# Optimization experiments

Measured on AMD Instinct MI355X. Metric: run time of the kernel, lower is better.

## Reference

```python
import jax, jax.numpy as jnp
import numpy as np
from math import sqrt

MEM_SIZE = 1024
MEM_DIM = 256


def setup_inputs() -> dict:
    key = jax.random.key(0)
    k1, k2, k3 = jax.random.split(key, 3)
    x = jax.random.normal(k1, (8, 256, 64, 64), dtype=jnp.float32)
    mask = jax.random.randint(k2, (8, 1, 64, 64), 0, 2).astype(jnp.bool_)
    mem = jax.random.normal(k3, (1, MEM_DIM, MEM_SIZE), dtype=jnp.float32)
    return {"x": x, "mask": mask, "mem": mem}


def reference(x, mask, mem):
    # masked-detach blend: x.detach() * ~mask + x * mask
    x = jnp.where(mask, x, jax.lax.stop_gradient(x))
    B, K, H, W = x.shape
    xf = x.reshape(B, K, H * W)            # (B, K, N)
    m = mem[0]                              # (K, M) with M = mem_size
    # logits = m_key @ x / sqrt(K)  -> (B, M, N)
    logits = jnp.einsum('km,bkn->bmn', m, xf) / sqrt(K)
    attn = jax.nn.softmax(logits, axis=1)   # softmax over memory axis
    # out = m @ attn -> (B, K, N)
    out = jnp.einsum('km,bmn->bkn', m, attn).reshape(B, K, H, W)
    return (out, logits)
```

## Files before the change

### kernel.cpp

```cpp
#include <hip/hip_runtime.h>
#include <stdint.h>


typedef __attribute__((ext_vector_type(8))) __bf16 bf16x8;
typedef __attribute__((ext_vector_type(4))) float f32x4;

#define BQ 8
#define KD 256
#define MD 1024
#define ND 4096
#define NT 64

__device__ __forceinline__ unsigned short bf16_rne(float f) {
    union { float f; uint32_t u; } c; c.f = f;
    uint32_t u = c.u;
    uint32_t r = (u + 0x7FFFu + ((u >> 16) & 1u)) >> 16;
    return (unsigned short)r;
}

__global__ void prep_mem(const float* __restrict__ mem,
                         unsigned short* __restrict__ mT,
                         unsigned short* __restrict__ mR) {
    const int k = blockIdx.x;
    const int t = threadIdx.x;
    float4 v = reinterpret_cast<const float4*>(mem + (size_t)k * MD)[t];
    unsigned short h0 = bf16_rne(v.x), h1 = bf16_rne(v.y),
                   h2 = bf16_rne(v.z), h3 = bf16_rne(v.w);
    reinterpret_cast<uint2*>(mR + (size_t)k * MD)[t] =
        make_uint2((uint32_t)h0 | ((uint32_t)h1 << 16),
                   (uint32_t)h2 | ((uint32_t)h3 << 16));
    const int mm = t * 4;
    mT[(size_t)(mm + 0) * KD + k] = h0;
    mT[(size_t)(mm + 1) * KD + k] = h1;
    mT[(size_t)(mm + 2) * KD + k] = h2;
    mT[(size_t)(mm + 3) * KD + k] = h3;
}

__global__ __launch_bounds__(1024, 4) void fused_attn_mem(
    const float* __restrict__ x,
    const unsigned short* __restrict__ mT,
    const unsigned short* __restrict__ mR,
    float* __restrict__ out,
    float* __restrict__ logits)
{
    extern __shared__ char lds[];
    float* red_max = (float*)(lds);
    float* red_sum = (float*)(lds + 4096);

    const int tid = threadIdx.x;
    const int w   = tid >> 6;
    const int l   = tid & 63;
    const int l15 = l & 15;
    const int l4  = l >> 4;

    const int bid = blockIdx.x;
    const int g   = bid & 7;
    const int j   = bid >> 3;
    const int strip = g * 8 + (j & 7);
    const int b     = j >> 3;
    const int n0    = strip * NT;

    {
        const float* xb = x + (size_t)b * KD * ND + n0;
        const int k  = tid >> 2;
        const int nh = (tid & 3) * 16;
        const float4* src = reinterpret_cast<const float4*>(xb + (size_t)k * ND + nh);
        float4 v0 = src[0], v1 = src[1], v2 = src[2], v3 = src[3];
        float vals[16] = {v0.x, v0.y, v0.z, v0.w, v1.x, v1.y, v1.z, v1.w,
                          v2.x, v2.y, v2.z, v2.w, v3.x, v3.y, v3.z, v3.w};
        #pragma unroll
        for (int jj = 0; jj < 16; ++jj) {
            const int n = nh + jj;
            const int off = n * 512 + (((k >> 3) ^ (n & 7)) << 4) + (k & 7) * 2;
            *(unsigned short*)(lds + off) = bf16_rne(vals[jj]);
        }
    }
    __syncthreads();

    f32x4 acc[4][4];
    #pragma unroll
    for (int rt = 0; rt < 4; ++rt)
        #pragma unroll
        for (int ct = 0; ct < 4; ++ct)
            acc[rt][ct] = (f32x4){0.f, 0.f, 0.f, 0.f};

    #pragma unroll
    for (int ks = 0; ks < 8; ++ks) {
        const int kk = ks * 32 + l4 * 8;
        bf16x8 bfr[4];
        #pragma unroll
        for (int ct = 0; ct < 4; ++ct) {
            const int n = ct * 16 + l15;
            const int off = n * 512 + (((kk >> 3) ^ (n & 7)) << 4);
            bfr[ct] = *(const bf16x8*)(lds + off);
        }
        #pragma unroll
        for (int rt = 0; rt < 4; ++rt) {
            const int row = w * 64 + rt * 16 + l15;
            const bf16x8 afr = *(const bf16x8*)(mT + (size_t)row * KD + kk);
            #pragma unroll
            for (int ct = 0; ct < 4; ++ct)
                acc[rt][ct] = __builtin_amdgcn_mfma_f32_16x16x32_bf16(afr, bfr[ct], acc[rt][ct], 0, 0, 0);
        }
    }

    float lmax[4] = {-3e38f, -3e38f, -3e38f, -3e38f};
    #pragma unroll
    for (int rt = 0; rt < 4; ++rt) {
        #pragma unroll
        for (int ct = 0; ct < 4; ++ct) {
            f32x4 v = acc[rt][ct] * 0.0625f;
            acc[rt][ct] = v;
            lmax[ct] = fmaxf(lmax[ct], fmaxf(fmaxf(v[0], v[1]), fmaxf(v[2], v[3])));
        }
    }

    {
        char* sw = lds + 32768 + w * 4608;
        float* lg = logits + (size_t)b * MD * ND + n0;
        #pragma unroll
        for (int rt = 0; rt < 4; ++rt) {
            #pragma unroll
            for (int ct = 0; ct < 4; ++ct) {
                const int n = ct * 16 + l15;
                #pragma unroll
                for (int r = 0; r < 4; ++r) {
                    const int mloc = l4 * 4 + r;
                    *(float*)(sw + mloc * 272 + n * 4) = acc[rt][ct][r];
                }
            }
            __asm__ volatile("s_waitcnt lgkmcnt(0)" ::: "memory");
            __builtin_amdgcn_sched_barrier(0);
            #pragma unroll
            for (int p = 0; p < 4; ++p) {
                const int mloc = p * 4 + l4;
                const f32x4 v = *(const f32x4*)(sw + mloc * 272 + l15 * 16);
                *(f32x4*)(lg + (size_t)(w * 64 + rt * 16 + mloc) * ND + l15 * 4) = v;
            }
            __asm__ volatile("s_waitcnt lgkmcnt(0)" ::: "memory");
            __builtin_amdgcn_sched_barrier(0);
        }
    }

    #pragma unroll
    for (int ct = 0; ct < 4; ++ct) {
        float m = lmax[ct];
        m = fmaxf(m, __shfl_xor(m, 16, 64));
        m = fmaxf(m, __shfl_xor(m, 32, 64));
        lmax[ct] = m;
    }
    __syncthreads();
    if (l < 16) {
        #pragma unroll
        for (int ct = 0; ct < 4; ++ct)
            red_max[(w * 4 + ct) * 16 + l] = lmax[ct];
    }
    __syncthreads();

    float cmax[4];
    #pragma unroll
    for (int ct = 0; ct < 4; ++ct) {
        float m = -3e38f;
        #pragma unroll
        for (int ww = 0; ww < 16; ++ww)
            m = fmaxf(m, red_max[(ww * 4 + ct) * 16 + l15]);
        cmax[ct] = m;
    }

    float lsum[4] = {0.f, 0.f, 0.f, 0.f};
    #pragma unroll
    for (int rt = 0; rt < 4; ++rt) {
        #pragma unroll
        for (int ct = 0; ct < 4; ++ct) {
            f32x4 v = acc[rt][ct];
            v[0] = __expf(v[0] - cmax[ct]);
            v[1] = __expf(v[1] - cmax[ct]);
            v[2] = __expf(v[2] - cmax[ct]);
            v[3] = __expf(v[3] - cmax[ct]);
            lsum[ct] += (v[0] + v[1]) + (v[2] + v[3]);
            acc[rt][ct] = v;
        }
    }
    #pragma unroll
    for (int ct = 0; ct < 4; ++ct) {
        float s = lsum[ct];
        s += __shfl_xor(s, 16, 64);
        s += __shfl_xor(s, 32, 64);
        lsum[ct] = s;
    }
    if (l < 16) {
        #pragma unroll
        for (int ct = 0; ct < 4; ++ct)
            red_sum[(w * 4 + ct) * 16 + l] = lsum[ct];
    }
    __syncthreads();

    float rs[4];
    #pragma unroll
    for (int ct = 0; ct < 4; ++ct) {
        float s = 0.f;
        #pragma unroll
        for (int ww = 0; ww < 16; ++ww)
            s += red_sum[(ww * 4 + ct) * 16 + l15];
        rs[ct] = 1.0f / s;
    }

    #pragma unroll
    for (int rt = 0; rt < 4; ++rt) {
        #pragma unroll
        for (int ct = 0; ct < 4; ++ct) {
            f32x4 v = acc[rt][ct];
            unsigned short h0 = bf16_rne(v[0] * rs[ct]);
            unsigned short h1 = bf16_rne(v[1] * rs[ct]);
            unsigned short h2 = bf16_rne(v[2] * rs[ct]);
            unsigned short h3 = bf16_rne(v[3] * rs[ct]);
            const int m0 = w * 64 + rt * 16 + l4 * 4;
            const int n  = ct * 16 + l15;
            const int off = 32768 + n * 2048 + (((m0 >> 3) ^ (n & 7)) << 4) + (m0 & 7) * 2;
            *(uint2*)(lds + off) = make_uint2((uint32_t)h0 | ((uint32_t)h1 << 16),
                                              (uint32_t)h2 | ((uint32_t)h3 << 16));
        }
    }
    __syncthreads();

    f32x4 acc2[4];
    #pragma unroll
    for (int ct = 0; ct < 4; ++ct)
        acc2[ct] = (f32x4){0.f, 0.f, 0.f, 0.f};

    const unsigned short* arow = mR + (size_t)(w * 16 + l15) * MD;
    #pragma unroll 4
    for (int ks = 0; ks < 32; ++ks) {
        const int mk = ks * 32 + l4 * 8;
        const bf16x8 a2 = *(const bf16x8*)(arow + mk);
        #pragma unroll
        for (int ct = 0; ct < 4; ++ct) {
            const int n = ct * 16 + l15;
            const int off = 32768 + n * 2048 + (((mk >> 3) ^ (n & 7)) << 4);
            const bf16x8 b2 = *(const bf16x8*)(lds + off);
            acc2[ct] = __builtin_amdgcn_mfma_f32_16x16x32_bf16(a2, b2, acc2[ct], 0, 0, 0);
        }
    }
    __syncthreads();

    {
        char* sw = lds + 32768 + w * 4608;
        float* ob = out + (size_t)b * KD * ND + n0;
        #pragma unroll
        for (int ct = 0; ct < 4; ++ct) {
            const int n = ct * 16 + l15;
            #pragma unroll
            for (int r = 0; r < 4; ++r) {
                const int rr = l4 * 4 + r;
                *(float*)(sw + rr * 272 + n * 4) = acc2[ct][r];
            }
        }
        __asm__ volatile("s_waitcnt lgkmcnt(0)" ::: "memory");
        __builtin_amdgcn_sched_barrier(0);
        #pragma unroll
        for (int p = 0; p < 4; ++p) {
            const int rr = p * 4 + l4;
            const f32x4 v = *(const f32x4*)(sw + rr * 272 + l15 * 16);
            *(f32x4*)(ob + (size_t)(w * 16 + rr) * ND + l15 * 4) = v;
        }
    }
}

extern "C" void kernel_launch(void* const* d_in, const int* in_sizes, int n_in,
                              void* d_out, int out_size, void* d_ws, size_t ws_size,
                              hipStream_t stream) {
    (void)in_sizes; (void)n_in; (void)out_size; (void)ws_size;
    const float* x   = (const float*)d_in[0];
    const float* mem = (const float*)d_in[2];

    float* out    = (float*)d_out;
    float* logits = (float*)d_out + (size_t)BQ * KD * ND;

    unsigned short* mT = (unsigned short*)d_ws;
    unsigned short* mR = mT + (size_t)MD * KD;

    static int lds_attr_set = 0;
    if (!lds_attr_set) {
        hipFuncSetAttribute(reinterpret_cast<const void*>(&fused_attn_mem),
                            hipFuncAttributeMaxDynamicSharedMemorySize, 163840);
        lds_attr_set = 1;
    }

    prep_mem<<<dim3(256), dim3(256), 0, stream>>>(mem, mT, mR);
    fused_attn_mem<<<dim3(BQ * (ND / NT)), dim3(1024), 163840, stream>>>(x, mT, mR, out, logits);
}
```

Baseline: 112.1 us.

## Widen column tile to 128 with two-pass attention GEMM and reorganized LDS

Doubles the per-block column tile from 64 to 128, halving the grid and halving how often each block re-reads the bf16 memory matrices from global/L2. The second GEMM now runs in two passes over halves of the memory axis so the bf16 attention tile fits in LDS. The max reduction moves ahead of the logits store, x is loaded with nontemporal loads, and the logits/out writes use 32-wide coalesced rows. In exchange, the accumulator array doubles in size, which raises register pressure and may cause spills, and the extra pass adds barriers.

```diff
diff --git a/kernel.cpp b/kernel.cpp
--- a/kernel.cpp
+++ b/kernel.cpp
@@ -9,7 +9,12 @@
 #define KD 256
 #define MD 1024
 #define ND 4096
-#define NT 64
+#define NT 128
+
+#define SCR_STRIDE 8448
+#define SCR_ROW    528
+#define RED_MAX_OFF 147456
+#define RED_SUM_OFF 155648
 
 __device__ __forceinline__ unsigned short bf16_rne(float f) {
     union { float f; uint32_t u; } c; c.f = f;
@@ -44,8 +49,8 @@
     float* __restrict__ logits)
 {
     extern __shared__ char lds[];
-    float* red_max = (float*)(lds);
-    float* red_sum = (float*)(lds + 4096);
+    float* red_max = (float*)(lds + RED_MAX_OFF);
+    float* red_sum = (float*)(lds + RED_SUM_OFF);
 
     const int tid = threadIdx.x;
     const int w   = tid >> 6;
@@ -53,43 +58,46 @@
     const int l15 = l & 15;
     const int l4  = l >> 4;
 
-    const int bid = blockIdx.x;
-    const int g   = bid & 7;
-    const int j   = bid >> 3;
-    const int strip = g * 8 + (j & 7);
-    const int b     = j >> 3;
-    const int n0    = strip * NT;
+    const int q   = blockIdx.x;
+    const int g   = q & 7;
+    const int j   = q >> 3;
+    const int b   = j >> 2;
+    const int sid = g * 4 + (j & 3);
+    const int n0  = sid * NT;
+
+    const float* xb = x + (size_t)b * KD * ND + n0;
+    float* lg = logits + (size_t)b * MD * ND + n0;
+    float* ob = out + (size_t)b * KD * ND + n0;
 
     {
-        const float* xb = x + (size_t)b * KD * ND + n0;
         const int k  = tid >> 2;
-        const int nh = (tid & 3) * 16;
-        const float4* src = reinterpret_cast<const float4*>(xb + (size_t)k * ND + nh);
-        float4 v0 = src[0], v1 = src[1], v2 = src[2], v3 = src[3];
-        float vals[16] = {v0.x, v0.y, v0.z, v0.w, v1.x, v1.y, v1.z, v1.w,
-                          v2.x, v2.y, v2.z, v2.w, v3.x, v3.y, v3.z, v3.w};
-        #pragma unroll
-        for (int jj = 0; jj < 16; ++jj) {
+        const int nh = (tid & 3) * 32;
+        const f32x4* src = reinterpret_cast<const f32x4*>(xb + (size_t)k * ND + nh);
+        f32x4 v[8];
+        #pragma unroll
+        for (int i = 0; i < 8; ++i) v[i] = __builtin_nontemporal_load(src + i);
+        #pragma unroll
+        for (int jj = 0; jj < 32; ++jj) {
             const int n = nh + jj;
             const int off = n * 512 + (((k >> 3) ^ (n & 7)) << 4) + (k & 7) * 2;
-            *(unsigned short*)(lds + off) = bf16_rne(vals[jj]);
+            *(unsigned short*)(lds + off) = bf16_rne(v[jj >> 2][jj & 3]);
         }
     }
     __syncthreads();
 
-    f32x4 acc[4][4];
+    f32x4 acc[4][8];
     #pragma unroll
     for (int rt = 0; rt < 4; ++rt)
         #pragma unroll
-        for (int ct = 0; ct < 4; ++ct)
+        for (int ct = 0; ct < 8; ++ct)
             acc[rt][ct] = (f32x4){0.f, 0.f, 0.f, 0.f};
 
     #pragma unroll
     for (int ks = 0; ks < 8; ++ks) {
         const int kk = ks * 32 + l4 * 8;
-        bf16x8 bfr[4];
-        #pragma unroll
-        for (int ct = 0; ct < 4; ++ct) {
+        bf16x8 bfr[8];
+        #pragma unroll
+        for (int ct = 0; ct < 8; ++ct) {
             const int n = ct * 16 + l15;
             const int off = n * 512 + (((kk >> 3) ^ (n & 7)) << 4);
             bfr[ct] = *(const bf16x8*)(lds + off);
@@ -99,79 +107,81 @@
             const int row = w * 64 + rt * 16 + l15;
             const bf16x8 afr = *(const bf16x8*)(mT + (size_t)row * KD + kk);
             #pragma unroll
-            for (int ct = 0; ct < 4; ++ct)
+            for (int ct = 0; ct < 8; ++ct)
                 acc[rt][ct] = __builtin_amdgcn_mfma_f32_16x16x32_bf16(afr, bfr[ct], acc[rt][ct], 0, 0, 0);
         }
     }
 
-    float lmax[4] = {-3e38f, -3e38f, -3e38f, -3e38f};
+    float lmax[8];
+    #pragma unroll
+    for (int ct = 0; ct < 8; ++ct) lmax[ct] = -3e38f;
     #pragma unroll
     for (int rt = 0; rt < 4; ++rt) {
         #pragma unroll
-        for (int ct = 0; ct < 4; ++ct) {
+        for (int ct = 0; ct < 8; ++ct) {
             f32x4 v = acc[rt][ct] * 0.0625f;
             acc[rt][ct] = v;
             lmax[ct] = fmaxf(lmax[ct], fmaxf(fmaxf(v[0], v[1]), fmaxf(v[2], v[3])));
         }
     }
+    #pragma unroll
+    for (int ct = 0; ct < 8; ++ct) {
+        float m = lmax[ct];
+        m = fmaxf(m, __shfl_xor(m, 16, 64));
+        m = fmaxf(m, __shfl_xor(m, 32, 64));
+        lmax[ct] = m;
+    }
+    if (l < 16) {
+        #pragma unroll
+        for (int ct = 0; ct < 8; ++ct)
+            red_max[(w * 8 + ct) * 16 + l] = lmax[ct];
+    }
+    __syncthreads();
+
+    float cmax[8];
+    #pragma unroll
+    for (int ct = 0; ct < 8; ++ct) {
+        float m = -3e38f;
+        #pragma unroll
+        for (int ww = 0; ww < 16; ++ww)
+            m = fmaxf(m, red_max[(ww * 8 + ct) * 16 + l15]);
+        cmax[ct] = m;
+    }
 
     {
-        char* sw = lds + 32768 + w * 4608;
-        float* lg = logits + (size_t)b * MD * ND + n0;
+        char* sw = lds + w * SCR_STRIDE;
         #pragma unroll
         for (int rt = 0; rt < 4; ++rt) {
             #pragma unroll
-            for (int ct = 0; ct < 4; ++ct) {
+            for (int ct = 0; ct < 8; ++ct) {
                 const int n = ct * 16 + l15;
                 #pragma unroll
                 for (int r = 0; r < 4; ++r) {
                     const int mloc = l4 * 4 + r;
-                    *(float*)(sw + mloc * 272 + n * 4) = acc[rt][ct][r];
+                    *(float*)(sw + mloc * SCR_ROW + n * 4) = acc[rt][ct][r];
                 }
             }
             __asm__ volatile("s_waitcnt lgkmcnt(0)" ::: "memory");
             __builtin_amdgcn_sched_barrier(0);
             #pragma unroll
-            for (int p = 0; p < 4; ++p) {
-                const int mloc = p * 4 + l4;
-                const f32x4 v = *(const f32x4*)(sw + mloc * 272 + l15 * 16);
-                *(f32x4*)(lg + (size_t)(w * 64 + rt * 16 + mloc) * ND + l15 * 4) = v;
+            for (int p = 0; p < 8; ++p) {
+                const int row = p * 2 + (l >> 5);
+                const int c   = l & 31;
+                const f32x4 v = *(const f32x4*)(sw + row * SCR_ROW + c * 16);
+                *(f32x4*)(lg + (size_t)(w * 64 + rt * 16 + row) * ND + c * 4) = v;
             }
             __asm__ volatile("s_waitcnt lgkmcnt(0)" ::: "memory");
             __builtin_amdgcn_sched_barrier(0);
         }
     }
 
-    #pragma unroll
-    for (int ct = 0; ct < 4; ++ct) {
-        float m = lmax[ct];
-        m = fmaxf(m, __shfl_xor(m, 16, 64));
-        m = fmaxf(m, __shfl_xor(m, 32, 64));
-        lmax[ct] = m;
-    }
-    __syncthreads();
-    if (l < 16) {
-        #pragma unroll
-        for (int ct = 0; ct < 4; ++ct)
-            red_max[(w * 4 + ct) * 16 + l] = lmax[ct];
-    }
-    __syncthreads();
-
-    float cmax[4];
-    #pragma unroll
-    for (int ct = 0; ct < 4; ++ct) {
-        float m = -3e38f;
-        #pragma unroll
-        for (int ww = 0; ww < 16; ++ww)
-            m = fmaxf(m, red_max[(ww * 4 + ct) * 16 + l15]);
-        cmax[ct] = m;
-    }
-
-    float lsum[4] = {0.f, 0.f, 0.f, 0.f};
+    float lsum[8];
+    #pragma unroll
+    for (int ct = 0; ct < 8; ++ct) lsum[ct] = 0.f;
     #pragma unroll
     for (int rt = 0; rt < 4; ++rt) {
         #pragma unroll
-        for (int ct = 0; ct < 4; ++ct) {
+        for (int ct = 0; ct < 8; ++ct) {
             f32x4 v = acc[rt][ct];
             v[0] = __expf(v[0] - cmax[ct]);
             v[1] = __expf(v[1] - cmax[ct]);
@@ -182,7 +192,7 @@
         }
     }
     #pragma unroll
-    for (int ct = 0; ct < 4; ++ct) {
+    for (int ct = 0; ct < 8; ++ct) {
         float s = lsum[ct];
         s += __shfl_xor(s, 16, 64);
         s += __shfl_xor(s, 32, 64);
@@ -190,78 +200,82 @@
     }
     if (l < 16) {
         #pragma unroll
-        for (int ct = 0; ct < 4; ++ct)
-            red_sum[(w * 4 + ct) * 16 + l] = lsum[ct];
+        for (int ct = 0; ct < 8; ++ct)
+            red_sum[(w * 8 + ct) * 16 + l] = lsum[ct];
     }
     __syncthreads();
 
-    float rs[4];
-    #pragma unroll
-    for (int ct = 0; ct < 4; ++ct) {
+    float rs[8];
+    #pragma unroll
+    for (int ct = 0; ct < 8; ++ct) {
         float s = 0.f;
         #pragma unroll
         for (int ww = 0; ww < 16; ++ww)
-            s += red_sum[(ww * 4 + ct) * 16 + l15];
+            s += red_sum[(ww * 8 + ct) * 16 + l15];
         rs[ct] = 1.0f / s;
     }
 
-    #pragma unroll
-    for (int rt = 0; rt < 4; ++rt) {
-        #pragma unroll
-        for (int ct = 0; ct < 4; ++ct) {
-            f32x4 v = acc[rt][ct];
-            unsigned short h0 = bf16_rne(v[0] * rs[ct]);
-            unsigned short h1 = bf16_rne(v[1] * rs[ct]);
-            unsigned short h2 = bf16_rne(v[2] * rs[ct]);
-            unsigned short h3 = bf16_rne(v[3] * rs[ct]);
-            const int m0 = w * 64 + rt * 16 + l4 * 4;
-            const int n  = ct * 16 + l15;
-            const int off = 32768 + n * 2048 + (((m0 >> 3) ^ (n & 7)) << 4) + (m0 & 7) * 2;
-            *(uint2*)(lds + off) = make_uint2((uint32_t)h0 | ((uint32_t)h1 << 16),
-                                              (uint32_t)h2 | ((uint32_t)h3 << 16));
-        }
-    }
-    __syncthreads();
-
-    f32x4 acc2[4];
-    #pragma unroll
-    for (int ct = 0; ct < 4; ++ct)
-        acc2[ct] = (f32x4){0.f, 0.f, 0.f, 0.f};
-
-    const unsigned short* arow = mR + (size_t)(w * 16 + l15) * MD;
-    #pragma unroll 4
-    for (int ks = 0; ks < 32; ++ks) {
-        const int mk = ks * 32 + l4 * 8;
-        const bf16x8 a2 = *(const bf16x8*)(arow + mk);
-        #pragma unroll
-        for (int ct = 0; ct < 4; ++ct) {
-            const int n = ct * 16 + l15;
-            const int off = 32768 + n * 2048 + (((mk >> 3) ^ (n & 7)) << 4);
-            const bf16x8 b2 = *(const bf16x8*)(lds + off);
-            acc2[ct] = __builtin_amdgcn_mfma_f32_16x16x32_bf16(a2, b2, acc2[ct], 0, 0, 0);
-        }
-    }
-    __syncthreads();
+    f32x4 acc2[8];
+    #pragma unroll
+    for (int ct = 0; ct < 8; ++ct) acc2[ct] = (f32x4){0.f, 0.f, 0.f, 0.f};
+
+    #pragma unroll
+    for (int pass = 0; pass < 2; ++pass) {
+        if ((w >> 3) == pass) {
+            #pragma unroll
+            for (int rt = 0; rt < 4; ++rt) {
+                #pragma unroll
+                for (int ct = 0; ct < 8; ++ct) {
+                    f32x4 v = acc[rt][ct];
+                    unsigned short h0 = bf16_rne(v[0] * rs[ct]);
+                    unsigned short h1 = bf16_rne(v[1] * rs[ct]);
+                    unsigned short h2 = bf16_rne(v[2] * rs[ct]);
+                    unsigned short h3 = bf16_rne(v[3] * rs[ct]);
+                    const int mloc = (w & 7) * 64 + rt * 16 + l4 * 4;
+                    const int n    = ct * 16 + l15;
+                    const int off  = n * 1024 + (((mloc >> 3) ^ (n & 7)) << 4) + (mloc & 7) * 2;
+                    *(uint2*)(lds + off) = make_uint2((uint32_t)h0 | ((uint32_t)h1 << 16),
+                                                      (uint32_t)h2 | ((uint32_t)h3 << 16));
+                }
+            }
+        }
+        __syncthreads();
+
+        const unsigned short* arow = mR + (size_t)(w * 16 + l15) * MD + pass * 512;
+        #pragma unroll 4
+        for (int ks = 0; ks < 16; ++ks) {
+            const int mk = ks * 32 + l4 * 8;
+            const bf16x8 a2 = *(const bf16x8*)(arow + mk);
+            #pragma unroll
+            for (int ct = 0; ct < 8; ++ct) {
+                const int n = ct * 16 + l15;
+                const int off = n * 1024 + (((mk >> 3) ^ (n & 7)) << 4);
+                const bf16x8 b2 = *(const bf16x8*)(lds + off);
+                acc2[ct] = __builtin_amdgcn_mfma_f32_16x16x32_bf16(a2, b2, acc2[ct], 0, 0, 0);
+            }
+        }
+        __syncthreads();
+    }
 
     {
-        char* sw = lds + 32768 + w * 4608;
-        float* ob = out + (size_t)b * KD * ND + n0;
-        #pragma unroll
-        for (int ct = 0; ct < 4; ++ct) {
+        char* sw = lds + w * SCR_STRIDE;
+        #pragma unroll
+        for (int ct = 0; ct < 8; ++ct) {
             const int n = ct * 16 + l15;
             #pragma unroll
             for (int r = 0; r < 4; ++r) {
                 const int rr = l4 * 4 + r;
-                *(float*)(sw + rr * 272 + n * 4) = acc2[ct][r];
+                *(float*)(sw + rr * SCR_ROW + n * 4) = acc2[ct][r];
             }
         }
         __asm__ volatile("s_waitcnt lgkmcnt(0)" ::: "memory");
         __builtin_amdgcn_sched_barrier(0);
         #pragma unroll
-        for (int p = 0; p < 4; ++p) {
-            const int rr = p * 4 + l4;
-            const f32x4 v = *(const f32x4*)(sw + rr * 272 + l15 * 16);
-            *(f32x4*)(ob + (size_t)(w * 16 + rr) * ND + l15 * 4) = v;
+        for (int p = 0; p < 8; ++p) {
+            const int row = p * 2 + (l >> 5);
+            const int c   = l & 31;
+            const f32x4 v = *(const f32x4*)(sw + row * SCR_ROW + c * 16);
+            *(f32x4*)(ob + (size_t)(w * 16 + row) * ND + c * 4) = v;
         }
     }
 }
@@ -281,8 +295,8 @@
 
     static int lds_attr_set = 0;
     if (!lds_attr_set) {
-        hipFuncSetAttribute(reinterpret_cast<const void*>(&fused_attn_mem),
-                            hipFuncAttributeMaxDynamicSharedMemorySize, 163840);
+        (void)hipFuncSetAttribute(reinterpret_cast<const void*>(&fused_attn_mem),
+                                  hipFuncAttributeMaxDynamicSharedMemorySize, 163840);
         lds_attr_set = 1;
     }
 
```

After: 321.2 us. 2.87x slower.
